# Performance work log

Hardware: AMD Instinct MI355X
Metric: run time of the kernel (lower is better)

The kernel has to match this reference:

```python
import jax, jax.numpy as jnp
import numpy as np

B, N, T, F_IN, U = 8192, 8, 12, 16, 64
H = U // 2


def setup_inputs():
    key = jax.random.key(0)
    ks = jax.random.split(key, 30)
    def w(k, shape, s=0.08):
        return jax.random.normal(k, shape, jnp.float32) * s
    return {
        "ts": jax.random.normal(ks[0], (B, T, F_IN), jnp.float32),
        "gts": jax.random.normal(ks[1], (B, N, T, F_IN), jnp.float32),
        "emb_w": w(ks[2], (H, F_IN)), "emb_b": w(ks[3], (H,)),
        "attQ_w": w(ks[4], (U, U)), "attQ_b": w(ks[5], (U,)),
        "attK_w": w(ks[6], (U, U)), "attK_b": w(ks[7], (U,)),
        "attV_w": w(ks[8], (U, U)), "attV_b": w(ks[9], (U,)),
        "attF_w": w(ks[10], (U, 2 * U)), "attF_b": w(ks[11], (U,)),
        "fuse1_w": w(ks[12], (U, 2 * U)), "fuse1_b": w(ks[13], (U,)),
        "enc_Wih": w(ks[14], (T, 4 * U, H)), "enc_Whh": w(ks[15], (T, 4 * U, U)),
        "enc_bih": w(ks[16], (T, 4 * U)), "enc_bhh": w(ks[17], (T, 4 * U)),
        "enc2_Wih": w(ks[18], (N, T, 4 * U, H)), "enc2_Whh": w(ks[19], (N, T, 4 * U, U)),
        "enc2_bih": w(ks[20], (N, T, 4 * U)), "enc2_bhh": w(ks[21], (N, T, 4 * U)),
        "mlp1_w": w(ks[22], (H, U)), "mlp1_b": w(ks[23], (H,)),
        "mlp2_w": w(ks[24], (1, H)), "mlp2_b": w(ks[25], (1,)),
    }


def _lstm(x, h, c, Wih, Whh, bih, bhh):
    # torch.nn.LSTMCell gate order: i, f, g, o
    g = x @ Wih.T + h @ Whh.T + bih + bhh
    i, f, gg, o = jnp.split(g, 4, axis=-1)
    c2 = jax.nn.sigmoid(f) * c + jax.nn.sigmoid(i) * jnp.tanh(gg)
    return jax.nn.sigmoid(o) * jnp.tanh(c2), c2


def _lstm_nodes(x, h, c, Wih, Whh, bih, bhh):
    # x: (B,N,in), h/c: (B,N,U), Wih: (N,4U,in), Whh: (N,4U,U) -- distinct cell per node
    g = (jnp.einsum('bni,nji->bnj', x, Wih)
         + jnp.einsum('bnh,njh->bnj', h, Whh)
         + bih[None] + bhh[None])
    i, f, gg, o = jnp.split(g, 4, axis=-1)
    c2 = jax.nn.sigmoid(f) * c + jax.nn.sigmoid(i) * jnp.tanh(gg)
    return jax.nn.sigmoid(o) * jnp.tanh(c2), c2


def _att(query, keys, Qw, Qb, Kw, Kb, Vw, Vb, Fw, Fb):
    # batched version of ATT.forward(norm=False): per-key scores -> softmax over keys
    q = query @ Qw.T + Qb                    # (B,U)
    k = keys @ Kw.T + Kb                     # (B,N,U)
    v = keys @ Vw.T + Vb                     # (B,N,U)
    p = jax.nn.softmax(jnp.einsum('bu,bnu->bn', q, k) / jnp.sqrt(jnp.float32(U)), axis=-1)
    ctx = jnp.einsum('bn,bnu->bu', p, v)
    return jax.nn.relu(jnp.concatenate([ctx, query], axis=-1) @ Fw.T + Fb)


def _forward(ts, gts, emb_w, emb_b, attQ_w, attQ_b, attK_w, attK_b, attV_w, attV_b,
             attF_w, attF_b, fuse1_w, fuse1_b, enc_Wih, enc_Whh, enc_bih, enc_bhh,
             enc2_Wih, enc2_Whh, enc2_bih, enc2_bhh, mlp1_w, mlp1_b, mlp2_w, mlp2_b):
    b = ts.shape[0]
    ts_e = ts @ emb_w.T + emb_b              # (B,T,H)
    gts_e = gts @ emb_w.T + emb_b            # (B,N,T,H)
    z = jnp.zeros((b, U), ts.dtype)
    zn = jnp.zeros((b, N, U), ts.dtype)

    # step 0: zero initial state; the original discards step-0 cell state (c reset to zeros)
    h_ts, _ = _lstm(ts_e[:, 0], z, z, enc_Wih[0], enc_Whh[0], enc_bih[0], enc_bhh[0])
    h_g, _ = _lstm_nodes(gts_e[:, :, 0], zn, zn, enc2_Wih[:, 0], enc2_Whh[:, 0], enc2_bih[:, 0], enc2_bhh[:, 0])
    h_ts_a = _att(h_ts, h_g, attQ_w, attQ_b, attK_w, attK_b, attV_w, attV_b, attF_w, attF_b)
    h_rep = jnp.broadcast_to(h_ts[:, None, :], h_g.shape)
    h_gts = jax.nn.relu(jnp.concatenate([h_g, h_rep], axis=-1) @ fuse1_w.T + fuse1_b)

    def step(carry, xs):
        h_ts, c_ts, h_ts_a, h_gts, c_gts = carry
        x_ts, x_g, Wih, Whh, bih, bhh, W2ih, W2hh, b2ih, b2hh = xs
        h_ts, c_ts = _lstm(x_ts, h_ts_a, c_ts, Wih, Whh, bih, bhh)
        h_g, c_gts = _lstm_nodes(x_g, h_gts, c_gts, W2ih, W2hh, b2ih, b2hh)
        h_ts_a = _att(h_ts, h_g, attQ_w, attQ_b, attK_w, attK_b, attV_w, attV_b, attF_w, attF_b)
        h_rep = jnp.broadcast_to(h_ts[:, None, :], h_g.shape)
        h_gts = jax.nn.relu(jnp.concatenate([h_g, h_rep], axis=-1) @ fuse1_w.T + fuse1_b)
        return (h_ts, c_ts, h_ts_a, h_gts, c_gts), None

    xs = (
        jnp.swapaxes(ts_e[:, 1:], 0, 1),                 # (T-1,B,H)
        jnp.transpose(gts_e[:, :, 1:], (2, 0, 1, 3)),     # (T-1,B,N,H)
        enc_Wih[1:], enc_Whh[1:], enc_bih[1:], enc_bhh[1:],
        jnp.swapaxes(enc2_Wih, 0, 1)[1:], jnp.swapaxes(enc2_Whh, 0, 1)[1:],
        jnp.swapaxes(enc2_bih, 0, 1)[1:], jnp.swapaxes(enc2_bhh, 0, 1)[1:],
    )
    carry = (h_ts, z, h_ts_a, h_gts, zn)
    (h_ts, c_ts, h_ts_a, h_gts, c_gts), _ = jax.lax.scan(step, carry, xs)

    # mlp (eval mode: dropout is identity): Linear -> ReLU -> Linear
    hid = jax.nn.relu(h_ts_a @ mlp1_w.T + mlp1_b)
    return hid @ mlp2_w.T + mlp2_b            # (B,1)


def reference(ts, gts, emb_w, emb_b, attQ_w, attQ_b, attK_w, attK_b, attV_w, attV_b,
              attF_w, attF_b, fuse1_w, fuse1_b, enc_Wih, enc_Whh, enc_bih, enc_bhh,
              enc2_Wih, enc2_Whh, enc2_bih, enc2_bhh, mlp1_w, mlp1_b, mlp2_w, mlp2_b):
    return _forward(ts, gts, emb_w, emb_b, attQ_w, attQ_b, attK_w, attK_b, attV_w, attV_b,
                    attF_w, attF_b, fuse1_w, fuse1_b, enc_Wih, enc_Whh, enc_bih, enc_bhh,
                    enc2_Wih, enc2_Whh, enc2_bih, enc2_bhh, mlp1_w, mlp1_b, mlp2_w, mlp2_b)
```

## Files before the change

kernel.cpp:

```cpp
#include <hip/hip_runtime.h>

#define T_SZ 12
#define R_WG 16
#define NTHR 512
#define NWG  512

typedef float  vf4 __attribute__((ext_vector_type(4)));
typedef int    vi4 __attribute__((ext_vector_type(4)));
typedef __bf16 vbf8 __attribute__((ext_vector_type(8)));

__device__ __forceinline__ float sigm(float x){ return 1.f/(1.f+__expf(-x)); }
__device__ __forceinline__ float tanh_f(float x){
  float e=__expf(2.f*x); return 1.f - 2.f/(e+1.f);
}
__device__ __forceinline__ unsigned short bf_hi(float f){
  return __builtin_bit_cast(unsigned short,(__bf16)f);
}
__device__ __forceinline__ float bf_f(unsigned short h){
  return __uint_as_float(((unsigned int)h)<<16);
}
__device__ __forceinline__ vf4 mfma16(vi4 a, vi4 b, vf4 c){
  return __builtin_amdgcn_mfma_f32_16x16x32_bf16(
      __builtin_bit_cast(vbf8,a), __builtin_bit_cast(vbf8,b), c, 0, 0, 0);
}
__device__ __forceinline__ vi4 g16(const char* p){ return *(const vi4*)p; }

__device__ __forceinline__ void a_read(const char* h9,int slot,int ks,int arow,int kb,vi4& Ah,vi4& Al){
  int blk=((ks<<2)+kb)^(arow&7);
  const char* p=h9+slot*4096+(arow*8+blk)*16;
  Ah=*(const vi4*)p; Al=*(const vi4*)(p+2048);
}
__device__ __forceinline__ void h9_w1(char* h9,int slot,int row,int k,float v){
  int off=slot*4096+(row*8+((k>>3)^(row&7)))*16+(k&7)*2;
  unsigned short hi=bf_hi(v);
  *(unsigned short*)(h9+off)=hi;
  *(unsigned short*)(h9+off+2048)=bf_hi(v-bf_f(hi));
}
__device__ __forceinline__ void h9_w2(char* h9,int slot,int row,int k0,float v0,float v1){
  int off=slot*4096+(row*8+((k0>>3)^(row&7)))*16+(k0&7)*2;
  unsigned short h0=bf_hi(v0),h1=bf_hi(v1);
  *(unsigned*)(h9+off)=(unsigned)h0|((unsigned)h1<<16);
  *(unsigned*)(h9+off+2048)=(unsigned)bf_hi(v0-bf_f(h0))|((unsigned)bf_hi(v1-bf_f(h1))<<16);
}
__device__ __forceinline__ void h9_w4c(char* h9,int slot,int row,int k0,vf4 v){
  int off=slot*4096+(row*8+((k0>>3)^(row&7)))*16+(k0&7)*2;
  unsigned short h0=bf_hi(v[0]),h1=bf_hi(v[1]),h2=bf_hi(v[2]),h3=bf_hi(v[3]);
  uint2 hv; hv.x=(unsigned)h0|((unsigned)h1<<16); hv.y=(unsigned)h2|((unsigned)h3<<16);
  *(uint2*)(h9+off)=hv;
  uint2 lv;
  lv.x=(unsigned)bf_hi(v[0]-bf_f(h0))|((unsigned)bf_hi(v[1]-bf_f(h1))<<16);
  lv.y=(unsigned)bf_hi(v[2]-bf_f(h2))|((unsigned)bf_hi(v[3]-bf_f(h3))<<16);
  *(uint2*)(h9+off+2048)=lv;
}
__device__ __forceinline__ float h9_rd(const char* h9,int slot,int row,int k){
  int off=slot*4096+(row*8+((k>>3)^(row&7)))*16+(k&7)*2;
  return bf_f(*(const unsigned short*)(h9+off))+bf_f(*(const unsigned short*)(h9+off+2048));
}

struct Ptrs {
  const unsigned short* Wm; const unsigned short* Wa; const unsigned short* Xf;
  const float* Fbp; const float* bqk; const float* f1b;
  const float* m1w; const float* m1b; const float* m2w; const float* m2b;
  float* out;
};

__global__ __launch_bounds__(NTHR,4) void fused_kernel(Ptrs P){
  __shared__ __align__(16) char  h9[77824];
  __shared__ __align__(16) float pbuf[128];

  const int tid=threadIdx.x;
  const int r0=blockIdx.x*R_WG;
  const int w=tid>>6, ln=tid&63;
  const bool w4=(w<4);
  const int arow=ln&15, kb=ln>>4;
  const int rowL=ln&15;
  const int uA=((2*w)>>2)*16 + (ln>>4)*4 + ((2*w)&3);
  const int ub=(w&3)*16 + (ln>>4)*4;
  const char* Wmb=(const char*)P.Wm;
  const char* awb=(const char*)P.Wa + ((size_t)(w&3))*4096 + (size_t)ln*16;
  const char* Xfb=(const char*)P.Xf + (size_t)(r0+arow)*9*24*32;
  float* qkf=(float*)(h9+10*4096);

  const vf4 bqk4=*(const vf4*)(P.bqk+ub);
  const vf4 bF4 =*(const vf4*)(P.Fbp+ub);
  const vf4 bf14=*(const vf4*)(P.f1b+ub);

  float cst[9][2];
  #pragma unroll
  for(int l=0;l<9;l++){ cst[l][0]=0.f; cst[l][1]=0.f; }

  for(int i=tid;i<77824/16;i+=NTHR) ((vi4*)h9)[i]=(vi4){0,0,0,0};
  __syncthreads();

  auto attn_gemm=[&](int cidx,int slot,vf4 acc)->vf4{
    const char* Wc=awb + (size_t)cidx*16384;
    vi4 Bh,Bl;
    vi4 W0=g16(Wc),W1=g16(Wc+1024),W2=g16(Wc+2048),W3=g16(Wc+3072);
    a_read(h9,slot,0,arow,kb,Bh,Bl);
    acc=mfma16(W0,Bh,acc); acc=mfma16(W0,Bl,acc); acc=mfma16(W1,Bh,acc);
    a_read(h9,slot,1,arow,kb,Bh,Bl);
    acc=mfma16(W2,Bh,acc); acc=mfma16(W2,Bl,acc); acc=mfma16(W3,Bh,acc);
    return acc;
  };

  for(int t=0;t<T_SZ;t++){
    #pragma unroll
    for(int l=0;l<9;l++){
      const int slotA=(l==0)?0:l;
      const int slotW=(l==0)?9:(10+l);
      const char* Wl=Wmb + (((size_t)(l*12+t)*8 + w)*12288) + (size_t)ln*16;
      vf4 a0={0,0,0,0},a1={0,0,0,0};
      vi4 Bh,Bl,Wh0,Wh1,Wl0,Wl1;
      Wh0=g16(Wl); Wh1=g16(Wl+1024); Wl0=g16(Wl+2048); Wl1=g16(Wl+3072);
      a_read(h9,slotA,0,arow,kb,Bh,Bl);
      a0=mfma16(Wh0,Bh,a0); a0=mfma16(Wh0,Bl,a0); a0=mfma16(Wl0,Bh,a0);
      a1=mfma16(Wh1,Bh,a1); a1=mfma16(Wh1,Bl,a1); a1=mfma16(Wl1,Bh,a1);
      {
        const char* Wk=Wl+4096;
        Wh0=g16(Wk); Wh1=g16(Wk+1024); Wl0=g16(Wk+2048); Wl1=g16(Wk+3072);
      }
      a_read(h9,slotA,1,arow,kb,Bh,Bl);
      a0=mfma16(Wh0,Bh,a0); a0=mfma16(Wh0,Bl,a0); a0=mfma16(Wl0,Bh,a0);
      a1=mfma16(Wh1,Bh,a1); a1=mfma16(Wh1,Bl,a1); a1=mfma16(Wl1,Bh,a1);
      {
        const char* Wk=Wl+8192;
        Wh0=g16(Wk); Wh1=g16(Wk+1024); Wl0=g16(Wk+2048); Wl1=g16(Wk+3072);
      }
      if(kb<2){
        const char* xp=Xfb + (size_t)(l*24 + t*2 + kb)*32;
        Bh=g16(xp); Bl=g16(xp+16);
      } else if(kb==2){ Bh=(vi4){0x3F80,0,0,0}; Bl=(vi4){0,0,0,0}; }
      else            { Bh=(vi4){0,0,0,0};     Bl=(vi4){0,0,0,0}; }
      a0=mfma16(Wh0,Bh,a0); a0=mfma16(Wh0,Bl,a0); a0=mfma16(Wl0,Bh,a0);
      a1=mfma16(Wh1,Bh,a1); a1=mfma16(Wh1,Bl,a1); a1=mfma16(Wl1,Bh,a1);
      {
        float iv=sigm(a0[0]), fv=sigm(a0[1]), gv=tanh_f(a0[2]), ov=sigm(a0[3]);
        float c20=fv*cst[l][0]+iv*gv;
        cst[l][0]=c20;
        float h0v=ov*tanh_f(c20);
        iv=sigm(a1[0]); fv=sigm(a1[1]); gv=tanh_f(a1[2]); ov=sigm(a1[3]);
        float c21=fv*cst[l][1]+iv*gv;
        cst[l][1]=c21;
        float h1v=ov*tanh_f(c21);
        h9_w2(h9,slotW,rowL,uA,h0v,h1v);
      }
    }
    __syncthreads();

    const bool dofuse=(t<T_SZ-1);
    vf4 g1,g2,g3,g4,g5,g6,g7,g8;
    #define FUSE(gn,slot) \
      a_read(h9,slot,0,arow,kb,Bh,Bl); \
      gn=mfma16(W0,Bh,gn); gn=mfma16(W0,Bl,gn); gn=mfma16(W1,Bh,gn); \
      a_read(h9,slot,1,arow,kb,Bh,Bl); \
      gn=mfma16(W2,Bh,gn); gn=mfma16(W2,Bl,gn); gn=mfma16(W3,Bh,gn);
    if(w4){
      vf4 aq=attn_gemm(0, 9, bqk4);
      *(vf4*)(qkf + rowL*64 + ub) = aq;
      if(dofuse){
        vf4 facc=attn_gemm(3, 9, bf14);
        const char* Wc=awb + (size_t)4*16384;
        vi4 W0=g16(Wc),W1=g16(Wc+1024),W2=g16(Wc+2048),W3=g16(Wc+3072);
        vi4 Bh,Bl;
        g1=facc;g2=facc;g3=facc;
        FUSE(g1,11) FUSE(g2,12) FUSE(g3,13)
      }
    } else if(dofuse){
      vf4 facc=attn_gemm(3, 9, bf14);
      const char* Wc=awb + (size_t)4*16384;
      vi4 W0=g16(Wc),W1=g16(Wc+1024),W2=g16(Wc+2048),W3=g16(Wc+3072);
      vi4 Bh,Bl;
      g4=facc;g5=facc;g6=facc;g7=facc;g8=facc;
      FUSE(g4,14) FUSE(g5,15) FUSE(g6,16) FUSE(g7,17) FUSE(g8,18)
    }
    #undef FUSE
    __syncthreads();
    {
      const int sub=tid&3, pair=tid>>2;
      const int rr=pair>>3, nn=pair&7;
      const char* hp=h9+(11+nn)*4096;
      float s=0.f;
      #pragma unroll
      for(int ii=0;ii<2;ii++){
        int kbl=sub*2+ii;
        int blk=kbl^(rr&7);
        const char* pp=hp+(rr*8+blk)*16;
        vi4 hv=*(const vi4*)pp;
        vi4 lv=*(const vi4*)(pp+2048);
        const vf4* qkp=(const vf4*)(qkf+rr*64+kbl*8);
        vf4 q0=qkp[0], q1=qkp[1];
        #pragma unroll
        for(int e=0;e<4;e++){
          unsigned hw=((const unsigned*)&hv)[e], lw=((const unsigned*)&lv)[e];
          float w0=__uint_as_float(hw<<16)+__uint_as_float(lw<<16);
          float w1=__uint_as_float(hw&0xffff0000u)+__uint_as_float(lw&0xffff0000u);
          float qa=(e<2)? q0[e*2] : q1[(e-2)*2];
          float qb=(e<2)? q0[e*2+1] : q1[(e-2)*2+1];
          s+=w0*qa+w1*qb;
        }
      }
      s+=__shfl_xor(s,1); s+=__shfl_xor(s,2);
      float mx=s;
      mx=fmaxf(mx,__shfl_xor(mx,4));
      mx=fmaxf(mx,__shfl_xor(mx,8));
      mx=fmaxf(mx,__shfl_xor(mx,16));
      float e=__expf(s-mx);
      float sm=e;
      sm+=__shfl_xor(sm,4); sm+=__shfl_xor(sm,8); sm+=__shfl_xor(sm,16);
      if(sub==0) pbuf[pair]=e/sm;
    }
    __syncthreads();
    {
      #pragma unroll
      for(int ri=0;ri<2;ri++){
        int row=w*2+ri;
        float sa=0.f;
        #pragma unroll
        for(int n=0;n<8;n++) sa+=pbuf[row*8+n]*h9_rd(h9,11+n,row,ln);
        h9_w1(h9,10,row,ln,sa);
      }
    }
    __syncthreads();
    #define WRX(gn,slot) \
      gn[0]=fmaxf(gn[0],0.f); gn[1]=fmaxf(gn[1],0.f); \
      gn[2]=fmaxf(gn[2],0.f); gn[3]=fmaxf(gn[3],0.f); \
      h9_w4c(h9,slot,rowL,ub,gn);
    if(w4){
      vf4 acA=attn_gemm(1, 10, bF4);
      acA=attn_gemm(2, 9, acA);
      acA[0]=fmaxf(acA[0],0.f); acA[1]=fmaxf(acA[1],0.f);
      acA[2]=fmaxf(acA[2],0.f); acA[3]=fmaxf(acA[3],0.f);
      h9_w4c(h9,0,rowL,ub,acA);
      if(dofuse){ WRX(g1,1) WRX(g2,2) WRX(g3,3) }
    } else if(dofuse){
      WRX(g4,4) WRX(g5,5) WRX(g6,6) WRX(g7,7) WRX(g8,8)
    }
    #undef WRX
    __syncthreads();
  }

  {
    float* hid=(float*)(h9+10*4096);
    int rr=tid>>5, ii=tid&31;
    float h=P.m1b[ii];
    for(int k=0;k<64;k++) h+=h9_rd(h9,0,rr,k)*P.m1w[(size_t)ii*64+k];
    hid[rr*32+ii]=fmaxf(h,0.f);
    __syncthreads();
    if(tid<R_WG){
      float s=P.m2b[0];
      for(int i=0;i<32;i++) s+=hid[tid*32+i]*P.m2w[i];
      P.out[r0+tid]=s;
    }
  }
}

__global__ void prep_wm(const float* eW, const float* eU, const float* e2W, const float* e2U,
                        const float* emb_w, const float* eb_ih, const float* eb_hh,
                        const float* e2b_ih, const float* e2b_hh, const float* emb_b,
                        unsigned short* dst){
  int id=blockIdx.x*256+threadIdx.x;
  if(id>=108*3*16*64) return;
  int lane=id&63;
  int q=id>>6;
  int wnt=q&15;
  int q2=q>>4;
  int ks=q2%3;
  int lt=q2/3;
  int LL=lt/12, t=lt%12;
  int c15=lane&15;
  int u=(wnt>>2)*16+(c15>>2)*4+(wnt&3);
  int gt=c15&3;
  int jg=gt*64+u;
  const float* Whh=(LL==0)? eU+((size_t)t*256+jg)*64 : e2U+(((size_t)(LL-1)*12+t)*256+jg)*64;
  const float* Wih=(LL==0)? eW+((size_t)t*256+jg)*32 : e2W+(((size_t)(LL-1)*12+t)*256+jg)*32;
  float bsum;
  {
    float bi=(LL==0)? eb_ih[t*256+jg] : e2b_ih[((LL-1)*12+t)*256+jg];
    float bh=(LL==0)? eb_hh[t*256+jg] : e2b_hh[((LL-1)*12+t)*256+jg];
    float s=bi+bh;
    for(int i=0;i<32;i++) s+=Wih[i]*emb_b[i];
    bsum=s;
  }
  int wv=wnt>>1, p=wnt&1;
  size_t base_hi=(((size_t)lt*8+wv)*12 + (4*ks+p  ))*512 + (size_t)lane*8;
  size_t base_lo=(((size_t)lt*8+wv)*12 + (4*ks+2+p))*512 + (size_t)lane*8;
  #pragma unroll
  for(int j=0;j<8;j++){
    int k=ks*32+(lane>>4)*8+j;
    float v;
    if(k<64) v=Whh[k];
    else if(k<80){
      int kx=k-64; float s=0.f;
      for(int i=0;i<32;i++) s+=Wih[i]*emb_w[i*16+kx];
      v=s;
    } else if(k==80) v=bsum;
    else v=0.f;
    unsigned short hi=bf_hi(v), lo=bf_hi(v-bf_f(hi));
    dst[base_hi+j]=hi;
    dst[base_lo+j]=lo;
  }
}

__global__ void prep_attw(const float* Qw, const float* Qb, const float* Kw,
                          const float* Vw, const float* Vb,
                          const float* Fw, const float* Fb, const float* f1w,
                          unsigned short* dst, float* Fbp, float* bqk){
  int id=blockIdx.x*256+threadIdx.x;
  if(id<5120){
    int cidx=id>>10;
    int rem=id&1023;
    int block=rem>>6;
    int lane=rem&63;
    int ks=(block>>1)&1, s=block&1;
    int cb=block>>2;
    int qq=(ks<<1)|s;
    int col=cb*16+(lane&15);
    size_t base=(((size_t)cidx*4+cb)*4 + qq)*512 + (size_t)lane*8;
    #pragma unroll
    for(int j=0;j<8;j++){
      int k=ks*32+(lane>>4)*8+j;
      float v;
      if(cidx==0){ float sv=0.f; for(int m=0;m<64;m++) sv+=Qw[m*64+k]*Kw[m*64+col]; v=sv*0.125f; }
      else if(cidx==1){ float sv=0.f; for(int m=0;m<64;m++) sv+=Fw[col*128+m]*Vw[m*64+k]; v=sv; }
      else if(cidx==2) v=Fw[col*128+64+k];
      else if(cidx==3) v=f1w[col*128+64+k];
      else             v=f1w[col*128+k];
      unsigned short hi=bf_hi(v);
      dst[base+j] = (s==0)? hi : bf_hi(v-bf_f(hi));
    }
  } else if(id<5184){
    int u=id-5120;
    float s=Fb[u];
    for(int m=0;m<64;m++) s+=Fw[u*128+m]*Vb[m];
    Fbp[u]=s;
  } else if(id<5248){
    int m=id-5184;
    float s=0.f;
    for(int u=0;u<64;u++) s+=Qb[u]*Kw[u*64+m];
    bqk[m]=s*0.125f;
  }
}

__global__ void prep_xf(const float* ts, const float* gts, unsigned short* xf){
  int id=blockIdx.x*256+threadIdx.x;
  if(id>=8192*9*24) return;
  int kb=id&1;
  int t=(id>>1)%12;
  int q=id/24;
  int src=q%9;
  int b=q/9;
  const float* s=(src==0)? ts+(size_t)b*192+(size_t)t*16+kb*8
                         : gts+(size_t)b*1536+(size_t)(src-1)*192+(size_t)t*16+kb*8;
  unsigned short* d=xf+(size_t)id*16;
  #pragma unroll
  for(int j=0;j<8;j++){
    float f=s[j];
    unsigned short hi=bf_hi(f);
    d[j]=hi;
    d[8+j]=bf_hi(f-bf_f(hi));
  }
}

extern "C" void kernel_launch(void* const* d_in, const int* in_sizes, int n_in,
                              void* d_out, int out_size, void* d_ws, size_t ws_size,
                              hipStream_t stream){
  const float* ts      =(const float*)d_in[0];
  const float* gts     =(const float*)d_in[1];
  const float* emb_w   =(const float*)d_in[2];
  const float* emb_b   =(const float*)d_in[3];
  const float* attQ_w  =(const float*)d_in[4];
  const float* attQ_b  =(const float*)d_in[5];
  const float* attK_w  =(const float*)d_in[6];
  const float* attV_w  =(const float*)d_in[8];
  const float* attV_b  =(const float*)d_in[9];
  const float* attF_w  =(const float*)d_in[10];
  const float* attF_b  =(const float*)d_in[11];
  const float* fuse1_w =(const float*)d_in[12];
  const float* fuse1_b =(const float*)d_in[13];
  const float* enc_Wih =(const float*)d_in[14];
  const float* enc_Whh =(const float*)d_in[15];
  const float* enc_bih =(const float*)d_in[16];
  const float* enc_bhh =(const float*)d_in[17];
  const float* enc2_Wih=(const float*)d_in[18];
  const float* enc2_Whh=(const float*)d_in[19];
  const float* enc2_bih=(const float*)d_in[20];
  const float* enc2_bhh=(const float*)d_in[21];
  const float* mlp1_w  =(const float*)d_in[22];
  const float* mlp1_b  =(const float*)d_in[23];
  const float* mlp2_w  =(const float*)d_in[24];
  const float* mlp2_b  =(const float*)d_in[25];

  char* ws=(char*)d_ws;
  size_t off=0;
  unsigned short* Wm=(unsigned short*)(ws+off); off+=(size_t)108*6*8192*2;
  unsigned short* Wa=(unsigned short*)(ws+off); off+=(size_t)5*8192*2;
  float* Fbp=(float*)(ws+off); off+=64*4;
  float* bqk=(float*)(ws+off); off+=64*4;
  unsigned short* Xf=(unsigned short*)(ws+off); off+=(size_t)8192*9*24*16*2;

  prep_wm<<<(108*3*16*64+255)/256,256,0,stream>>>(enc_Wih,enc_Whh,enc2_Wih,enc2_Whh,emb_w,
                                                  enc_bih,enc_bhh,enc2_bih,enc2_bhh,emb_b,Wm);
  prep_attw<<<21,256,0,stream>>>(attQ_w,attQ_b,attK_w,attV_w,attV_b,attF_w,attF_b,fuse1_w,
                                 Wa,Fbp,bqk);
  prep_xf<<<(8192*9*24+255)/256,256,0,stream>>>(ts,gts,Xf);

  Ptrs P;
  P.Wm=Wm; P.Wa=Wa; P.Xf=Xf;
  P.Fbp=Fbp; P.bqk=bqk; P.f1b=fuse1_b;
  P.m1w=mlp1_w; P.m1b=mlp1_b; P.m2w=mlp2_w; P.m2b=mlp2_b;
  P.out=(float*)d_out;

  fused_kernel<<<NWG,NTHR,0,stream>>>(P);
}
```

Baseline: 432.2 us.

## Double workgroup size to 16 waves and split per-wave recurrent work

The block grows from 8 to 16 waves. Each wave now computes a single 16-column MFMA gate tile per LSTM layer instead of two, and the fuse GEMMs are spread over four wave roles. Attention scoring uses 8 lanes per pair and the weighted sum handles one row per wave. The aim is to cut the serial per-wave latency of the recurrence by using more waves per workgroup, at the cost of higher occupancy pressure (launch bounds 1024 threads with min 8) and 64 KB+ of LDS per block, which may limit residency. Fuse role work is also unbalanced (1/2/3/2 slots).

```diff
diff --git a/kernel.cpp b/kernel.cpp
--- a/kernel.cpp
+++ b/kernel.cpp
@@ -2,7 +2,7 @@
 
 #define T_SZ 12
 #define R_WG 16
-#define NTHR 512
+#define NTHR 1024
 #define NWG  512
 
 typedef float  vf4 __attribute__((ext_vector_type(4)));
@@ -35,12 +35,6 @@
   unsigned short hi=bf_hi(v);
   *(unsigned short*)(h9+off)=hi;
   *(unsigned short*)(h9+off+2048)=bf_hi(v-bf_f(hi));
-}
-__device__ __forceinline__ void h9_w2(char* h9,int slot,int row,int k0,float v0,float v1){
-  int off=slot*4096+(row*8+((k0>>3)^(row&7)))*16+(k0&7)*2;
-  unsigned short h0=bf_hi(v0),h1=bf_hi(v1);
-  *(unsigned*)(h9+off)=(unsigned)h0|((unsigned)h1<<16);
-  *(unsigned*)(h9+off+2048)=(unsigned)bf_hi(v0-bf_f(h0))|((unsigned)bf_hi(v1-bf_f(h1))<<16);
 }
 __device__ __forceinline__ void h9_w4c(char* h9,int slot,int row,int k0,vf4 v){
   int off=slot*4096+(row*8+((k0>>3)^(row&7)))*16+(k0&7)*2;
@@ -64,20 +58,20 @@
   float* out;
 };
 
-__global__ __launch_bounds__(NTHR,4) void fused_kernel(Ptrs P){
+__global__ __launch_bounds__(NTHR,8) void fused_kernel(Ptrs P){
   __shared__ __align__(16) char  h9[77824];
   __shared__ __align__(16) float pbuf[128];
 
   const int tid=threadIdx.x;
   const int r0=blockIdx.x*R_WG;
   const int w=tid>>6, ln=tid&63;
-  const bool w4=(w<4);
+  const int role=w>>2, cb=w&3;
   const int arow=ln&15, kb=ln>>4;
   const int rowL=ln&15;
-  const int uA=((2*w)>>2)*16 + (ln>>4)*4 + ((2*w)&3);
-  const int ub=(w&3)*16 + (ln>>4)*4;
+  const int u_w=(w>>2)*16 + kb*4 + (w&3);
+  const int ub=cb*16 + kb*4;
   const char* Wmb=(const char*)P.Wm;
-  const char* awb=(const char*)P.Wa + ((size_t)(w&3))*4096 + (size_t)ln*16;
+  const char* awb=(const char*)P.Wa + ((size_t)cb)*4096 + (size_t)ln*16;
   const char* Xfb=(const char*)P.Xf + (size_t)(r0+arow)*9*24*32;
   float* qkf=(float*)(h9+10*4096);
 
@@ -85,9 +79,9 @@
   const vf4 bF4 =*(const vf4*)(P.Fbp+ub);
   const vf4 bf14=*(const vf4*)(P.f1b+ub);
 
-  float cst[9][2];
+  float cst[9];
   #pragma unroll
-  for(int l=0;l<9;l++){ cst[l][0]=0.f; cst[l][1]=0.f; }
+  for(int l=0;l<9;l++) cst[l]=0.f;
 
   for(int i=tid;i<77824/16;i+=NTHR) ((vi4*)h9)[i]=(vi4){0,0,0,0};
   __syncthreads();
@@ -108,81 +102,66 @@
     for(int l=0;l<9;l++){
       const int slotA=(l==0)?0:l;
       const int slotW=(l==0)?9:(10+l);
-      const char* Wl=Wmb + (((size_t)(l*12+t)*8 + w)*12288) + (size_t)ln*16;
-      vf4 a0={0,0,0,0},a1={0,0,0,0};
-      vi4 Bh,Bl,Wh0,Wh1,Wl0,Wl1;
-      Wh0=g16(Wl); Wh1=g16(Wl+1024); Wl0=g16(Wl+2048); Wl1=g16(Wl+3072);
+      const char* Wl=Wmb + (((size_t)(l*12+t)*8 + (w>>1))*12288) + (size_t)(w&1)*1024 + (size_t)ln*16;
+      vf4 a0={0,0,0,0};
+      vi4 Bh,Bl,Wh,Wlo;
+      Wh=g16(Wl); Wlo=g16(Wl+2048);
       a_read(h9,slotA,0,arow,kb,Bh,Bl);
-      a0=mfma16(Wh0,Bh,a0); a0=mfma16(Wh0,Bl,a0); a0=mfma16(Wl0,Bh,a0);
-      a1=mfma16(Wh1,Bh,a1); a1=mfma16(Wh1,Bl,a1); a1=mfma16(Wl1,Bh,a1);
-      {
-        const char* Wk=Wl+4096;
-        Wh0=g16(Wk); Wh1=g16(Wk+1024); Wl0=g16(Wk+2048); Wl1=g16(Wk+3072);
-      }
+      a0=mfma16(Wh,Bh,a0); a0=mfma16(Wh,Bl,a0); a0=mfma16(Wlo,Bh,a0);
+      Wh=g16(Wl+4096); Wlo=g16(Wl+6144);
       a_read(h9,slotA,1,arow,kb,Bh,Bl);
-      a0=mfma16(Wh0,Bh,a0); a0=mfma16(Wh0,Bl,a0); a0=mfma16(Wl0,Bh,a0);
-      a1=mfma16(Wh1,Bh,a1); a1=mfma16(Wh1,Bl,a1); a1=mfma16(Wl1,Bh,a1);
-      {
-        const char* Wk=Wl+8192;
-        Wh0=g16(Wk); Wh1=g16(Wk+1024); Wl0=g16(Wk+2048); Wl1=g16(Wk+3072);
-      }
+      a0=mfma16(Wh,Bh,a0); a0=mfma16(Wh,Bl,a0); a0=mfma16(Wlo,Bh,a0);
+      Wh=g16(Wl+8192); Wlo=g16(Wl+10240);
       if(kb<2){
         const char* xp=Xfb + (size_t)(l*24 + t*2 + kb)*32;
         Bh=g16(xp); Bl=g16(xp+16);
       } else if(kb==2){ Bh=(vi4){0x3F80,0,0,0}; Bl=(vi4){0,0,0,0}; }
       else            { Bh=(vi4){0,0,0,0};     Bl=(vi4){0,0,0,0}; }
-      a0=mfma16(Wh0,Bh,a0); a0=mfma16(Wh0,Bl,a0); a0=mfma16(Wl0,Bh,a0);
-      a1=mfma16(Wh1,Bh,a1); a1=mfma16(Wh1,Bl,a1); a1=mfma16(Wl1,Bh,a1);
+      a0=mfma16(Wh,Bh,a0); a0=mfma16(Wh,Bl,a0); a0=mfma16(Wlo,Bh,a0);
       {
         float iv=sigm(a0[0]), fv=sigm(a0[1]), gv=tanh_f(a0[2]), ov=sigm(a0[3]);
-        float c20=fv*cst[l][0]+iv*gv;
-        cst[l][0]=c20;
-        float h0v=ov*tanh_f(c20);
-        iv=sigm(a1[0]); fv=sigm(a1[1]); gv=tanh_f(a1[2]); ov=sigm(a1[3]);
-        float c21=fv*cst[l][1]+iv*gv;
-        cst[l][1]=c21;
-        float h1v=ov*tanh_f(c21);
-        h9_w2(h9,slotW,rowL,uA,h0v,h1v);
+        float c2=fv*cst[l]+iv*gv;
+        cst[l]=c2;
+        h9_w1(h9,slotW,rowL,u_w,ov*tanh_f(c2));
       }
     }
     __syncthreads();
 
     const bool dofuse=(t<T_SZ-1);
-    vf4 g1,g2,g3,g4,g5,g6,g7,g8;
-    #define FUSE(gn,slot) \
+    vf4 gA,gB,gC;
+    #define FUSE(gn,slot) { \
       a_read(h9,slot,0,arow,kb,Bh,Bl); \
       gn=mfma16(W0,Bh,gn); gn=mfma16(W0,Bl,gn); gn=mfma16(W1,Bh,gn); \
       a_read(h9,slot,1,arow,kb,Bh,Bl); \
-      gn=mfma16(W2,Bh,gn); gn=mfma16(W2,Bl,gn); gn=mfma16(W3,Bh,gn);
-    if(w4){
+      gn=mfma16(W2,Bh,gn); gn=mfma16(W2,Bl,gn); gn=mfma16(W3,Bh,gn); }
+    if(role==0){
       vf4 aq=attn_gemm(0, 9, bqk4);
       *(vf4*)(qkf + rowL*64 + ub) = aq;
       if(dofuse){
-        vf4 facc=attn_gemm(3, 9, bf14);
+        vf4 fa=attn_gemm(3, 9, bf14);
         const char* Wc=awb + (size_t)4*16384;
         vi4 W0=g16(Wc),W1=g16(Wc+1024),W2=g16(Wc+2048),W3=g16(Wc+3072);
         vi4 Bh,Bl;
-        g1=facc;g2=facc;g3=facc;
-        FUSE(g1,11) FUSE(g2,12) FUSE(g3,13)
+        gA=fa; FUSE(gA,11)
       }
     } else if(dofuse){
-      vf4 facc=attn_gemm(3, 9, bf14);
+      vf4 fa=attn_gemm(3, 9, bf14);
       const char* Wc=awb + (size_t)4*16384;
       vi4 W0=g16(Wc),W1=g16(Wc+1024),W2=g16(Wc+2048),W3=g16(Wc+3072);
       vi4 Bh,Bl;
-      g4=facc;g5=facc;g6=facc;g7=facc;g8=facc;
-      FUSE(g4,14) FUSE(g5,15) FUSE(g6,16) FUSE(g7,17) FUSE(g8,18)
+      if(role==1){ gA=fa; FUSE(gA,12) gB=fa; FUSE(gB,13) }
+      else if(role==2){ gA=fa; FUSE(gA,14) gB=fa; FUSE(gB,15) gC=fa; FUSE(gC,16) }
+      else { gA=fa; FUSE(gA,17) gB=fa; FUSE(gB,18) }
     }
     #undef FUSE
     __syncthreads();
     {
-      const int sub=tid&3, pair=tid>>2;
+      const int sub=tid&7, pair=tid>>3;
       const int rr=pair>>3, nn=pair&7;
       const char* hp=h9+(11+nn)*4096;
       float s=0.f;
-      #pragma unroll
-      for(int ii=0;ii<2;ii++){
-        int kbl=sub*2+ii;
+      {
+        int kbl=sub;
         int blk=kbl^(rr&7);
         const char* pp=hp+(rr*8+blk)*16;
         vi4 hv=*(const vi4*)pp;
@@ -199,41 +178,39 @@
           s+=w0*qa+w1*qb;
         }
       }
-      s+=__shfl_xor(s,1); s+=__shfl_xor(s,2);
+      s+=__shfl_xor(s,1); s+=__shfl_xor(s,2); s+=__shfl_xor(s,4);
       float mx=s;
-      mx=fmaxf(mx,__shfl_xor(mx,4));
       mx=fmaxf(mx,__shfl_xor(mx,8));
       mx=fmaxf(mx,__shfl_xor(mx,16));
+      mx=fmaxf(mx,__shfl_xor(mx,32));
       float e=__expf(s-mx);
       float sm=e;
-      sm+=__shfl_xor(sm,4); sm+=__shfl_xor(sm,8); sm+=__shfl_xor(sm,16);
+      sm+=__shfl_xor(sm,8); sm+=__shfl_xor(sm,16); sm+=__shfl_xor(sm,32);
       if(sub==0) pbuf[pair]=e/sm;
     }
     __syncthreads();
     {
+      float sa=0.f;
       #pragma unroll
-      for(int ri=0;ri<2;ri++){
-        int row=w*2+ri;
-        float sa=0.f;
-        #pragma unroll
-        for(int n=0;n<8;n++) sa+=pbuf[row*8+n]*h9_rd(h9,11+n,row,ln);
-        h9_w1(h9,10,row,ln,sa);
-      }
-    }
-    __syncthreads();
-    #define WRX(gn,slot) \
+      for(int n=0;n<8;n++) sa+=pbuf[w*8+n]*h9_rd(h9,11+n,w,ln);
+      h9_w1(h9,10,w,ln,sa);
+    }
+    __syncthreads();
+    #define WRX(gn,slot) { \
       gn[0]=fmaxf(gn[0],0.f); gn[1]=fmaxf(gn[1],0.f); \
       gn[2]=fmaxf(gn[2],0.f); gn[3]=fmaxf(gn[3],0.f); \
-      h9_w4c(h9,slot,rowL,ub,gn);
-    if(w4){
+      h9_w4c(h9,slot,rowL,ub,gn); }
+    if(role==0){
       vf4 acA=attn_gemm(1, 10, bF4);
       acA=attn_gemm(2, 9, acA);
       acA[0]=fmaxf(acA[0],0.f); acA[1]=fmaxf(acA[1],0.f);
       acA[2]=fmaxf(acA[2],0.f); acA[3]=fmaxf(acA[3],0.f);
       h9_w4c(h9,0,rowL,ub,acA);
-      if(dofuse){ WRX(g1,1) WRX(g2,2) WRX(g3,3) }
+      if(dofuse){ WRX(gA,1) }
     } else if(dofuse){
-      WRX(g4,4) WRX(g5,5) WRX(g6,6) WRX(g7,7) WRX(g8,8)
+      if(role==1){ WRX(gA,2) WRX(gB,3) }
+      else if(role==2){ WRX(gA,4) WRX(gB,5) WRX(gC,6) }
+      else { WRX(gA,7) WRX(gB,8) }
     }
     #undef WRX
     __syncthreads();
@@ -241,10 +218,12 @@
 
   {
     float* hid=(float*)(h9+10*4096);
-    int rr=tid>>5, ii=tid&31;
-    float h=P.m1b[ii];
-    for(int k=0;k<64;k++) h+=h9_rd(h9,0,rr,k)*P.m1w[(size_t)ii*64+k];
-    hid[rr*32+ii]=fmaxf(h,0.f);
+    if(tid<512){
+      int rr=tid>>5, ii=tid&31;
+      float h=P.m1b[ii];
+      for(int k=0;k<64;k++) h+=h9_rd(h9,0,rr,k)*P.m1w[(size_t)ii*64+k];
+      hid[rr*32+ii]=fmaxf(h,0.f);
+    }
     __syncthreads();
     if(tid<R_WG){
       float s=P.m2b[0];
```

Measured after the change: 689.5 us. 1.6x slower.
